# Kernel optimization log

Measured on AMD Instinct MI355X. Metric: run time of the kernel, lower is better.

## Reference

```python
import jax, jax.numpy as jnp
import numpy as np

B, S, DM, H, FF, BLOCK, R = 2, 4096, 768, 12, 3072, 64, 3
NB = S // BLOCK  # 64 blocks


def _layer_norm(x, g, b, eps=1e-5):
    mu = jnp.mean(x, -1, keepdims=True)
    var = jnp.var(x, -1, keepdims=True)
    return (x - mu) * jax.lax.rsqrt(var + eps) * g + b


def _bigbird_attn(x, rand_attn, Wq, bq, Wk, bk, Wv, bv):
    b_, s_, dm = x.shape
    h_ = H
    d = dm // h_
    n = s_ // BLOCK
    r = rand_attn.shape[-1]
    scale = 1.0 / np.sqrt(d).astype(np.float32)

    def heads(y):  # [B,S,DM] -> [B,H,n,block,D]
        return y.reshape(b_, s_, h_, d).transpose(0, 2, 1, 3).reshape(b_, h_, n, BLOCK, d)

    qb = heads(x @ Wq + bq)
    kb = heads(x @ Wk + bk)
    vb = heads(x @ Wv + bv)
    k_full = kb.reshape(b_, h_, s_, d)
    v_full = vb.reshape(b_, h_, s_, d)

    # gather random key/value blocks per head: [B,H,n-2,r*block,D]
    gather = jax.vmap(lambda zh, idx: zh[:, idx], in_axes=(1, 0), out_axes=1)
    gk = gather(kb, rand_attn).reshape(b_, h_, n - 2, r * BLOCK, d)
    gv = gather(vb, rand_attn).reshape(b_, h_, n - 2, r * BLOCK, d)

    def attend(q, k, v):
        s = jnp.einsum('...qd,...kd->...qk', q, k) * scale
        a = jax.nn.softmax(s, axis=-1)
        return jnp.einsum('...qk,...kd->...qd', a, v)

    # first block: full attention over all keys
    c_first = attend(qb[:, :, 0], k_full, v_full)

    # second block: blocks 0,1,2 + last block + random blocks
    k2 = jnp.concatenate([kb[:, :, 0], kb[:, :, 1], kb[:, :, 2], kb[:, :, -1], gk[:, :, 0]], axis=2)
    v2 = jnp.concatenate([vb[:, :, 0], vb[:, :, 1], vb[:, :, 2], vb[:, :, -1], gv[:, :, 0]], axis=2)
    c_second = attend(qb[:, :, 1], k2, v2)

    # middle blocks 2..n-3: global-first + 3-block sliding window + random + global-last
    m = n - 4
    qm = qb[:, :, 2:-2]  # [B,H,m,block,D]

    def band(z):  # sliding window of 3 blocks around each middle block
        return jnp.concatenate([z[:, :, 1:-3], z[:, :, 2:-2], z[:, :, 3:-1]], axis=3)

    bc = lambda z: jnp.broadcast_to(z[:, :, None], (b_, h_, m, BLOCK, d))
    km = jnp.concatenate([bc(kb[:, :, 0]), band(kb), gk[:, :, 1:-1], bc(kb[:, :, -1])], axis=3)
    vm = jnp.concatenate([bc(vb[:, :, 0]), band(vb), gv[:, :, 1:-1], bc(vb[:, :, -1])], axis=3)
    c_mid = attend(qm, km, vm)  # [B,H,m,block,D]

    # second-to-last block: block 0 + last three blocks + random blocks
    kp = jnp.concatenate([kb[:, :, 0], kb[:, :, -3], kb[:, :, -2], kb[:, :, -1], gk[:, :, -1]], axis=2)
    vp = jnp.concatenate([vb[:, :, 0], vb[:, :, -3], vb[:, :, -2], vb[:, :, -1], gv[:, :, -1]], axis=2)
    c_pen = attend(qb[:, :, -2], kp, vp)

    # last block: full attention over all keys
    c_last = attend(qb[:, :, -1], k_full, v_full)

    ctx = jnp.concatenate([c_first[:, :, None], c_second[:, :, None], c_mid,
                           c_pen[:, :, None], c_last[:, :, None]], axis=2)
    return ctx.reshape(b_, h_, s_, d).transpose(0, 2, 1, 3).reshape(b_, s_, dm)


def setup_inputs() -> dict:
    key = jax.random.key(0)
    ks = jax.random.split(key, 16)
    p = lambda k, shape: (jax.random.normal(k, shape, jnp.float32) * 0.02)
    return {
        'x': jax.random.normal(ks[0], (B, S, DM), jnp.float32),
        'rand_attn': jax.random.randint(ks[1], (H, NB - 2, R), 0, NB - 2, jnp.int32),
        'Wq': p(ks[2], (DM, DM)), 'bq': jnp.zeros((DM,), jnp.float32),
        'Wk': p(ks[3], (DM, DM)), 'bk': jnp.zeros((DM,), jnp.float32),
        'Wv': p(ks[4], (DM, DM)), 'bv': jnp.zeros((DM,), jnp.float32),
        'ln1_g': jnp.ones((DM,), jnp.float32), 'ln1_b': jnp.zeros((DM,), jnp.float32),
        'W1': p(ks[5], (DM, FF)), 'b1': jnp.zeros((FF,), jnp.float32),
        'W2': p(ks[6], (FF, DM)), 'b2': jnp.zeros((DM,), jnp.float32),
        'ln2_g': jnp.ones((DM,), jnp.float32), 'ln2_b': jnp.zeros((DM,), jnp.float32),
    }


def reference(x, rand_attn, Wq, bq, Wk, bk, Wv, bv, ln1_g, ln1_b, W1, b1, W2, b2, ln2_g, ln2_b):
    attn = _bigbird_attn(x, rand_attn, Wq, bq, Wk, bk, Wv, bv)
    h = _layer_norm(attn + x, ln1_g, ln1_b)  # dropout is identity in eval
    ffn = jax.nn.gelu(h @ W1 + b1, approximate=False) @ W2 + b2
    return _layer_norm(ffn + h, ln2_g, ln2_b)
```

## Files before the change

### kernel.cpp

```cpp
#include <hip/hip_runtime.h>
#include <cmath>


typedef unsigned short bf;
typedef __attribute__((ext_vector_type(8))) short bf16x8;
typedef __attribute__((ext_vector_type(4))) float f32x4;

__device__ __forceinline__ float bf2f(bf u) { return __uint_as_float(((unsigned)u) << 16); }
__device__ __forceinline__ bf f2bf(float f) {
  unsigned x = __float_as_uint(f);
  x += 0x7FFFu + ((x >> 16) & 1u);
  return (bf)(x >> 16);
}

__device__ __forceinline__ void gload16(const bf* g, char* lds) {
  __builtin_amdgcn_global_load_lds(
      (const __attribute__((address_space(1))) void*)g,
      (__attribute__((address_space(3))) void*)lds, 16, 0, 0);
}

__global__ __launch_bounds__(256) void cvt_x_k(const float* __restrict__ X,
                                               bf* __restrict__ xb)
{
  size_t i = ((size_t)blockIdx.x * 256 + threadIdx.x) * 8;
  float4 f0 = *(const float4*)&X[i];
  float4 f1 = *(const float4*)&X[i + 4];
  *(ushort4*)&xb[i]     = make_ushort4(f2bf(f0.x), f2bf(f0.y), f2bf(f0.z), f2bf(f0.w));
  *(ushort4*)&xb[i + 4] = make_ushort4(f2bf(f1.x), f2bf(f1.y), f2bf(f1.z), f2bf(f1.w));
}

__global__ __launch_bounds__(256) void tconv_k(const float* __restrict__ W,
                                               bf* __restrict__ Wt, int K, int N)
{
  __shared__ float tile[64][65];
  const int t = threadIdx.x;
  const int bn = blockIdx.x * 64, bk = blockIdx.y * 64;
  const int r = t >> 2, c0 = (t & 3) * 16;
  #pragma unroll
  for (int i = 0; i < 4; ++i) {
    float4 f = *(const float4*)&W[(size_t)(bk + r) * N + bn + c0 + i * 4];
    tile[r][c0 + i*4 + 0] = f.x; tile[r][c0 + i*4 + 1] = f.y;
    tile[r][c0 + i*4 + 2] = f.z; tile[r][c0 + i*4 + 3] = f.w;
  }
  __syncthreads();
  #pragma unroll
  for (int i = 0; i < 4; ++i) {
    int c = c0 + i * 4;
    ushort4 u = make_ushort4(f2bf(tile[c + 0][r]), f2bf(tile[c + 1][r]),
                             f2bf(tile[c + 2][r]), f2bf(tile[c + 3][r]));
    *(ushort4*)&Wt[(size_t)(bn + r) * K + bk + c] = u;
  }
}

template <int BN, typename TC>
__global__ __launch_bounds__(256) void gl_gemm_k(
    const bf* __restrict__ A, const bf* __restrict__ Bt,
    const float* __restrict__ bias, TC* __restrict__ C,
    int M, int N, int K, int ldbt, int ep)
{
  constexpr int NJ = BN / 32;
  __shared__ char smem[16384 + BN * 128];
  char* sA = smem;
  char* sB = smem + 16384;
  const int t = threadIdx.x;
  const int bm = blockIdx.y * 128, bn = blockIdx.x * BN;
  const int lane = t & 63, wid = t >> 6;
  const int wm = wid >> 1, wn = wid & 1;
  const int fr = lane & 15, fq = lane >> 4;
  const int lr = lane >> 3, lk = (lane & 7) * 8;

  f32x4 acc[4][NJ];
  #pragma unroll
  for (int i = 0; i < 4; ++i)
    #pragma unroll
    for (int j = 0; j < NJ; ++j) acc[i][j] = (f32x4){0.f, 0.f, 0.f, 0.f};

  for (int k0 = 0; k0 < K; k0 += 64) {
    #pragma unroll
    for (int c = 0; c < 4; ++c) {
      int chunk = wid * 4 + c;
      int row = chunk * 8 + lr;
      gload16(A + (size_t)(bm + row) * K + k0 + lk, sA + chunk * 1024);
    }
    #pragma unroll
    for (int c = 0; c < NJ; ++c) {
      int chunk = wid * NJ + c;
      int col = chunk * 8 + lr;
      gload16(Bt + (size_t)(bn + col) * ldbt + k0 + lk, sB + chunk * 1024);
    }
    __syncthreads();
    #pragma unroll
    for (int kk = 0; kk < 2; ++kk) {
      const int kb = kk * 64 + fq * 16;
      bf16x8 a[4], b[NJ];
      #pragma unroll
      for (int i = 0; i < 4; ++i)
        a[i] = *(const bf16x8*)(sA + (wm * 64 + i * 16 + fr) * 128 + kb);
      #pragma unroll
      for (int j = 0; j < NJ; ++j)
        b[j] = *(const bf16x8*)(sB + (wn * (BN / 2) + j * 16 + fr) * 128 + kb);
      #pragma unroll
      for (int i = 0; i < 4; ++i)
        #pragma unroll
        for (int j = 0; j < NJ; ++j)
          acc[i][j] = __builtin_amdgcn_mfma_f32_16x16x32_bf16(a[i], b[j], acc[i][j], 0, 0, 0);
    }
    __syncthreads();
  }
  #pragma unroll
  for (int j = 0; j < NJ; ++j) {
    int col = bn + wn * (BN / 2) + j * 16 + fr;
    float bias_v = bias ? bias[col] : 0.f;
    #pragma unroll
    for (int i = 0; i < 4; ++i) {
      int row0 = bm + wm * 64 + i * 16 + fq * 4;
      #pragma unroll
      for (int r = 0; r < 4; ++r) {
        float v = acc[i][j][r] + bias_v;
        if (ep == 1) v = 0.5f * v * (1.0f + erff(v * 0.70710678118654752f));
        if constexpr (sizeof(TC) == 2) C[(size_t)(row0 + r) * N + col] = f2bf(v);
        else                           C[(size_t)(row0 + r) * N + col] = v;
      }
    }
  }
}

__global__ __launch_bounds__(256) void qkv_gl_k(
    const bf* __restrict__ A, const bf* __restrict__ Bt,
    const float* __restrict__ bq, const float* __restrict__ bk,
    const float* __restrict__ bv,
    bf* __restrict__ Qo, bf* __restrict__ Ko, bf* __restrict__ Vo)
{
  __shared__ char smem[32768];
  char* sA = smem;
  char* sB = smem + 16384;
  const int t = threadIdx.x;
  const int bm = blockIdx.y * 128, bn = blockIdx.x * 128;
  const int lane = t & 63, wid = t >> 6;
  const int wm = wid >> 1, wn = wid & 1;
  const int fr = lane & 15, fq = lane >> 4;
  const int lr = lane >> 3, lk = (lane & 7) * 8;
  const int K = 768;

  f32x4 acc[4][4];
  #pragma unroll
  for (int i = 0; i < 4; ++i)
    #pragma unroll
    for (int j = 0; j < 4; ++j) acc[i][j] = (f32x4){0.f, 0.f, 0.f, 0.f};

  for (int k0 = 0; k0 < K; k0 += 64) {
    #pragma unroll
    for (int c = 0; c < 4; ++c) {
      int chunk = wid * 4 + c;
      gload16(A + (size_t)(bm + chunk * 8 + lr) * K + k0 + lk, sA + chunk * 1024);
    }
    #pragma unroll
    for (int c = 0; c < 4; ++c) {
      int chunk = wid * 4 + c;
      gload16(Bt + (size_t)(bn + chunk * 8 + lr) * K + k0 + lk, sB + chunk * 1024);
    }
    __syncthreads();
    #pragma unroll
    for (int kk = 0; kk < 2; ++kk) {
      const int kb = kk * 64 + fq * 16;
      bf16x8 a[4], b[4];
      #pragma unroll
      for (int i = 0; i < 4; ++i)
        a[i] = *(const bf16x8*)(sA + (wm * 64 + i * 16 + fr) * 128 + kb);
      #pragma unroll
      for (int j = 0; j < 4; ++j)
        b[j] = *(const bf16x8*)(sB + (wn * 64 + j * 16 + fr) * 128 + kb);
      #pragma unroll
      for (int i = 0; i < 4; ++i)
        #pragma unroll
        for (int j = 0; j < 4; ++j)
          acc[i][j] = __builtin_amdgcn_mfma_f32_16x16x32_bf16(a[i], b[j], acc[i][j], 0, 0, 0);
    }
    __syncthreads();
  }
  const int seg = bn / 768;
  const int cb  = bn - seg * 768;
  bf* dst = (seg == 0) ? Qo : ((seg == 1) ? Ko : Vo);
  const float* bias = (seg == 0) ? bq : ((seg == 1) ? bk : bv);
  #pragma unroll
  for (int j = 0; j < 4; ++j) {
    int col = cb + wn * 64 + j * 16 + fr;
    float bias_v = bias[col];
    #pragma unroll
    for (int i = 0; i < 4; ++i) {
      int row0 = bm + wm * 64 + i * 16 + fq * 4;
      #pragma unroll
      for (int r = 0; r < 4; ++r)
        dst[(size_t)(row0 + r) * 768 + col] = f2bf(acc[i][j][r] + bias_v);
    }
  }
}

__device__ __forceinline__ void stage_kv(char* bK, char* bVT,
    int kkey, int kd0, int vkey, int w,
    uint4 k0, uint4 k1, uint4 v0, uint4 v1)
{
  const int sw = (kkey & 7) << 4;
  *(uint4*)(bK + kkey * 128 + ((2 * kd0) ^ sw))      = k0;
  *(uint4*)(bK + kkey * 128 + ((2 * kd0 + 16) ^ sw)) = k1;
  union { uint4 q; unsigned short s[8]; } a, c;
  a.q = v0; c.q = v1;
  #pragma unroll
  for (int i = 0; i < 8; ++i) {
    int d = w * 16 + i;
    *(unsigned short*)(bVT + d * 128 + ((2 * vkey) ^ ((d & 7) << 4))) = a.s[i];
  }
  #pragma unroll
  for (int i = 0; i < 8; ++i) {
    int d = w * 16 + 8 + i;
    *(unsigned short*)(bVT + d * 128 + ((2 * vkey) ^ ((d & 7) << 4))) = c.s[i];
  }
}

__global__ __launch_bounds__(256) void attn5_kernel(
    const bf* __restrict__ Q, const bf* __restrict__ K,
    const bf* __restrict__ V, const int* __restrict__ rnd,
    float* __restrict__ ctx, float* __restrict__ part, int nseg)
{
  __shared__ char sQP[8192];
  __shared__ char sKV[2][16384];
  __shared__ int klist[8];
  const int t = threadIdx.x;
  const int lane = t & 63, w = t >> 6;
  const int fr = lane & 15, fq = lane >> 4;
  const int wg = blockIdx.x;
  const int nheavy = 48 * nseg;
  const bool heavy = wg < nheavy;
  int b, h, n, nkb, seg = 0, hidx = 0, segBase = 0;
  if (heavy) {
    hidx = wg / nseg; seg = wg - hidx * nseg;
    n = (hidx & 1) ? 63 : 0;
    int bh = hidx >> 1; h = bh % 12; b = bh / 12;
    nkb = 64 / nseg; segBase = seg * nkb;
  } else {
    int idx = wg - nheavy;
    n = 1 + (idx % 62);
    int bh = idx / 62; h = bh % 12; b = bh / 12;
    nkb = (n == 1 || n == 62) ? 7 : 8;
    if (t == 0) {
      int cnt = 0;
      if (n == 1)       { klist[0]=0; klist[1]=1;  klist[2]=2;  klist[3]=63; cnt=4; }
      else if (n == 62) { klist[0]=0; klist[1]=61; klist[2]=62; klist[3]=63; cnt=4; }
      else              { klist[0]=0; klist[1]=n-1; klist[2]=n; klist[3]=n+1; cnt=4; }
      for (int j = 0; j < 3; ++j) klist[cnt++] = rnd[(h * 62 + (n - 1)) * 3 + j];
      if (n != 1 && n != 62) klist[cnt++] = 63;
    }
  }
  const size_t qbase = ((size_t)b * 4096 + (size_t)n * 64) * 768 + h * 64;

  {
    int row = t >> 2, d0 = (t & 3) * 16;
    const bf* qp = &Q[qbase + (size_t)row * 768 + d0];
    #pragma unroll
    for (int i = 0; i < 2; ++i) {
      int off = row * 128 + ((2 * (d0 + 8 * i)) ^ ((row & 7) << 4));
      *(uint4*)(sQP + off) = *(const uint4*)(qp + 8 * i);
    }
  }
  __syncthreads();
  bf16x8 qf[2];
  {
    int row = w * 16 + fr;
    qf[0] = *(const bf16x8*)(sQP + row * 128 + ((2 * (fq * 8))      ^ ((row & 7) << 4)));
    qf[1] = *(const bf16x8*)(sQP + row * 128 + ((2 * (32 + fq * 8)) ^ ((row & 7) << 4)));
  }

  const int kkey = t >> 2, kd0 = (t & 3) * 16;
  const int vkey = lane;

  uint4 pk0, pk1, pv0, pv1;
  {
    int kb = heavy ? segBase : klist[0];
    size_t kbase = ((size_t)b * 4096 + (size_t)kb * 64) * 768 + h * 64;
    const bf* kp = &K[kbase + (size_t)kkey * 768 + kd0];
    pk0 = *(const uint4*)kp;  pk1 = *(const uint4*)(kp + 8);
    const bf* vp = &V[kbase + (size_t)vkey * 768 + w * 16];
    pv0 = *(const uint4*)vp;  pv1 = *(const uint4*)(vp + 8);
  }
  stage_kv(sKV[0], sKV[0] + 8192, kkey, kd0, vkey, w, pk0, pk1, pv0, pv1);

  float m_r[4] = {-1e30f, -1e30f, -1e30f, -1e30f};
  float l_r[4] = {0.f, 0.f, 0.f, 0.f};
  f32x4 acc_o[4];
  #pragma unroll
  for (int j = 0; j < 4; ++j) acc_o[j] = (f32x4){0.f, 0.f, 0.f, 0.f};

  for (int ib = 0; ib < nkb; ++ib) {
    char* bK  = sKV[ib & 1];
    char* bVT = bK + 8192;
    const bool pfv = (ib + 1 < nkb);
    if (pfv) {
      int kb = heavy ? (segBase + ib + 1) : klist[ib + 1];
      size_t kbase = ((size_t)b * 4096 + (size_t)kb * 64) * 768 + h * 64;
      const bf* kp = &K[kbase + (size_t)kkey * 768 + kd0];
      pk0 = *(const uint4*)kp;  pk1 = *(const uint4*)(kp + 8);
      const bf* vp = &V[kbase + (size_t)vkey * 768 + w * 16];
      pv0 = *(const uint4*)vp;  pv1 = *(const uint4*)(vp + 8);
    }
    __syncthreads();
    f32x4 s4[4];
    #pragma unroll
    for (int j = 0; j < 4; ++j) s4[j] = (f32x4){0.f, 0.f, 0.f, 0.f};
    __builtin_amdgcn_s_setprio(1);
    #pragma unroll
    for (int kk = 0; kk < 2; ++kk) {
      #pragma unroll
      for (int j = 0; j < 4; ++j) {
        int key = j * 16 + fr;
        bf16x8 kf = *(const bf16x8*)(bK + key * 128 + ((2 * (kk * 32 + fq * 8)) ^ ((key & 7) << 4)));
        s4[j] = __builtin_amdgcn_mfma_f32_16x16x32_bf16(qf[kk], kf, s4[j], 0, 0, 0);
      }
    }
    __builtin_amdgcn_s_setprio(0);
    #pragma unroll
    for (int j = 0; j < 4; ++j) s4[j] *= 0.125f;
    float c_r[4];
    #pragma unroll
    for (int r = 0; r < 4; ++r) {
      float mx = fmaxf(fmaxf(s4[0][r], s4[1][r]), fmaxf(s4[2][r], s4[3][r]));
      #pragma unroll
      for (int m = 1; m < 16; m <<= 1) mx = fmaxf(mx, __shfl_xor(mx, m, 64));
      float mn = fmaxf(mx, m_r[r]);
      float c  = __expf(m_r[r] - mn);
      float p0 = __expf(s4[0][r] - mn), p1 = __expf(s4[1][r] - mn);
      float p2 = __expf(s4[2][r] - mn), p3 = __expf(s4[3][r] - mn);
      s4[0][r] = p0; s4[1][r] = p1; s4[2][r] = p2; s4[3][r] = p3;
      float sum = p0 + p1 + p2 + p3;
      #pragma unroll
      for (int m = 1; m < 16; m <<= 1) sum += __shfl_xor(sum, m, 64);
      l_r[r] = l_r[r] * c + sum;
      m_r[r] = mn;
      c_r[r] = c;
    }
    #pragma unroll
    for (int j = 0; j < 4; ++j)
      #pragma unroll
      for (int r = 0; r < 4; ++r) acc_o[j][r] *= c_r[r];
    #pragma unroll
    for (int r = 0; r < 4; ++r) {
      int prow = w * 16 + fq * 4 + r;
      int rs = prow * 128, sw = (prow & 7) << 4;
      #pragma unroll
      for (int j = 0; j < 4; ++j)
        *(unsigned short*)(sQP + rs + ((2 * (j * 16 + fr)) ^ sw)) = f2bf(s4[j][r]);
    }
    if (pfv)
      stage_kv(sKV[(ib & 1) ^ 1], sKV[(ib & 1) ^ 1] + 8192, kkey, kd0, vkey, w,
               pk0, pk1, pv0, pv1);
    __builtin_amdgcn_s_setprio(1);
    #pragma unroll
    for (int kk = 0; kk < 2; ++kk) {
      int prow = w * 16 + fr;
      bf16x8 pf8 = *(const bf16x8*)(sQP + prow * 128 + ((2 * (kk * 32 + fq * 8)) ^ ((prow & 7) << 4)));
      #pragma unroll
      for (int j = 0; j < 4; ++j) {
        int col = j * 16 + fr;
        bf16x8 vf = *(const bf16x8*)(bVT + col * 128 + ((2 * (kk * 32 + fq * 8)) ^ ((col & 7) << 4)));
        acc_o[j] = __builtin_amdgcn_mfma_f32_16x16x32_bf16(pf8, vf, acc_o[j], 0, 0, 0);
      }
    }
    __builtin_amdgcn_s_setprio(0);
  }
  if (heavy && nseg > 1) {
    float* pb = part + ((size_t)hidx * nseg + seg) * 4224;
    int row0 = w * 16 + fq * 4;
    #pragma unroll
    for (int r = 0; r < 4; ++r) {
      int row = row0 + r;
      if (fr == 0) { pb[4096 + row] = m_r[r]; pb[4160 + row] = l_r[r]; }
      #pragma unroll
      for (int j = 0; j < 4; ++j)
        pb[row * 64 + j * 16 + fr] = acc_o[j][r];
    }
  } else {
    int row0 = w * 16 + fq * 4;
    #pragma unroll
    for (int r = 0; r < 4; ++r) {
      float inv = 1.f / l_r[r];
      size_t rowoff = qbase + (size_t)(row0 + r) * 768;
      #pragma unroll
      for (int j = 0; j < 4; ++j)
        ctx[rowoff + j * 16 + fr] = acc_o[j][r] * inv;
    }
  }
}

__global__ __launch_bounds__(256) void attn_combine_k(
    const float* __restrict__ part, float* __restrict__ ctx)
{
  const int hidx = blockIdx.x;
  const int t = threadIdx.x;
  const int n = (hidx & 1) ? 63 : 0;
  const int bh = hidx >> 1;
  const int h = bh % 12, b = bh / 12;
  const size_t qbase = ((size_t)b * 4096 + (size_t)n * 64) * 768 + h * 64;
  const int r = t >> 2, d0 = (t & 3) * 16;
  const float* pb = part + (size_t)hidx * 8 * 4224;
  float mi[8], li[8], m = -1e30f;
  #pragma unroll
  for (int i = 0; i < 8; ++i) {
    mi[i] = pb[i * 4224 + 4096 + r];
    li[i] = pb[i * 4224 + 4160 + r];
    m = fmaxf(m, mi[i]);
  }
  float w8[8], L = 0.f;
  #pragma unroll
  for (int i = 0; i < 8; ++i) { w8[i] = __expf(mi[i] - m); L += li[i] * w8[i]; }
  float inv = 1.f / L;
  #pragma unroll
  for (int dd = 0; dd < 4; ++dd) {
    int d = d0 + dd * 4;
    float4 o = {0.f, 0.f, 0.f, 0.f};
    #pragma unroll
    for (int i = 0; i < 8; ++i) {
      float4 p = *(const float4*)&pb[i * 4224 + r * 64 + d];
      o.x = fmaf(w8[i], p.x, o.x); o.y = fmaf(w8[i], p.y, o.y);
      o.z = fmaf(w8[i], p.z, o.z); o.w = fmaf(w8[i], p.w, o.w);
    }
    o.x *= inv; o.y *= inv; o.z *= inv; o.w *= inv;
    *(float4*)&ctx[qbase + (size_t)r * 768 + d] = o;
  }
}

template <typename TR, typename TO>
__global__ __launch_bounds__(256) void ln_kernel(
    const float* __restrict__ a, const TR* __restrict__ res,
    const float* __restrict__ g, const float* __restrict__ bb,
    TO* __restrict__ out)
{
  const int row = blockIdx.x, t = threadIdx.x;
  __shared__ float buf[768];
  __shared__ float rs[4], rss[4];
  const size_t base = (size_t)row * 768;
  float s = 0.f, ss = 0.f;
  for (int c = t; c < 768; c += 256) {
    float rv;
    if constexpr (sizeof(TR) == 2) rv = bf2f(res[base + c]);
    else                           rv = res[base + c];
    float v = a[base + c] + rv;
    buf[c] = v;
    s += v;
    ss = fmaf(v, v, ss);
  }
  #pragma unroll
  for (int off = 32; off > 0; off >>= 1) {
    s  += __shfl_down(s, off, 64);
    ss += __shfl_down(ss, off, 64);
  }
  if ((t & 63) == 0) { rs[t >> 6] = s; rss[t >> 6] = ss; }
  __syncthreads();
  float S  = rs[0] + rs[1] + rs[2] + rs[3];
  float SS = rss[0] + rss[1] + rss[2] + rss[3];
  float mu  = S * (1.f / 768.f);
  float var = SS * (1.f / 768.f) - mu * mu;
  float inv = rsqrtf(var + 1e-5f);
  for (int c = t; c < 768; c += 256) {
    float v = (buf[c] - mu) * inv * g[c] + bb[c];
    if constexpr (sizeof(TO) == 2) out[base + c] = f2bf(v);
    else                           out[base + c] = v;
  }
}

extern "C" void kernel_launch(void* const* d_in, const int* in_sizes, int n_in,
                              void* d_out, int out_size, void* d_ws, size_t ws_size,
                              hipStream_t stream)
{
  const float* x   = (const float*)d_in[0];
  const int*   rnd = (const int*)d_in[1];
  const float* Wq  = (const float*)d_in[2];
  const float* bq  = (const float*)d_in[3];
  const float* Wk  = (const float*)d_in[4];
  const float* bk  = (const float*)d_in[5];
  const float* Wv  = (const float*)d_in[6];
  const float* bv  = (const float*)d_in[7];
  const float* g1  = (const float*)d_in[8];
  const float* be1 = (const float*)d_in[9];
  const float* W1  = (const float*)d_in[10];
  const float* b1  = (const float*)d_in[11];
  const float* W2  = (const float*)d_in[12];
  const float* b2  = (const float*)d_in[13];
  const float* g2  = (const float*)d_in[14];
  const float* be2 = (const float*)d_in[15];
  float* out = (float*)d_out;

  char* W = (char*)d_ws;
  bf* w1t   = (bf*)(W);
  bf* w2t   = (bf*)(W + 4718592);
  bf* Kb    = (bf*)(W + 9437184);
  bf* wqkv  = (bf*)(W + 22020096);
  bf* xb    = (bf*)(W + 25559040);
  bf* Qb    = (bf*)(W + 38141952);
  bf* Vb    = (bf*)(W + 50724864);
  float* part = (float*)(W + 63307776);
  bf* f1    = (bf*)(W + 22020096);
  bf* h1    = Kb;
  float* ctx = out;
  float* f2  = out;

  dim3 blk(256);
  cvt_x_k<<<dim3(3072), blk, 0, stream>>>(x, xb);
  tconv_k<<<dim3(12, 12), blk, 0, stream>>>(Wq, wqkv,               768, 768);
  tconv_k<<<dim3(12, 12), blk, 0, stream>>>(Wk, wqkv + 589824,      768, 768);
  tconv_k<<<dim3(12, 12), blk, 0, stream>>>(Wv, wqkv + 2 * 589824,  768, 768);
  tconv_k<<<dim3(48, 12), blk, 0, stream>>>(W1, w1t,  768, 3072);
  tconv_k<<<dim3(12, 48), blk, 0, stream>>>(W2, w2t, 3072,  768);
  qkv_gl_k<<<dim3(18, 64), blk, 0, stream>>>(xb, wqkv, bq, bk, bv, Qb, Kb, Vb);
  attn5_kernel<<<dim3(48 * 8 + 2 * 12 * 62), blk, 0, stream>>>(
      Qb, Kb, Vb, rnd, ctx, part, 8);
  attn_combine_k<<<dim3(48), blk, 0, stream>>>(part, ctx);
  ln_kernel<float, bf><<<dim3(8192), blk, 0, stream>>>(ctx, x, g1, be1, h1);
  gl_gemm_k<128, bf><<<dim3(24, 64), blk, 0, stream>>>(
      h1, w1t, b1, f1, 8192, 3072, 768, 768, 1);
  gl_gemm_k<64, float><<<dim3(12, 64), blk, 0, stream>>>(
      f1, w2t, b2, f2, 8192, 768, 3072, 3072, 0);
  ln_kernel<bf, float><<<dim3(8192), blk, 0, stream>>>(f2, h1, g2, be2, out);
}
```

Measured before the change: 330.6 us.

## Double-buffer LDS in GEMM kernels and widen the W2 GEMM tile

Both GEMM kernels (the generic one and the fused QKV projection) now keep two LDS stages. The global-to-LDS load for the next K tile is issued before the MFMA work on the current tile, with one waitcnt and barrier per iteration instead of two syncthreads. Priority is raised around the MFMA block, and sched_barriers keep the compiler from reordering across stages. The FFN down-projection also switches from BN=64 to BN=128, halving its grid to 384 blocks, which trades fewer redundant A loads for lower occupancy and parallelism.

New measurement: 301.2 us. -8.9%, faster.

```diff
diff --git a/kernel.cpp b/kernel.cpp
--- a/kernel.cpp
+++ b/kernel.cpp
@@ -59,9 +59,9 @@
     int M, int N, int K, int ldbt, int ep)
 {
   constexpr int NJ = BN / 32;
-  __shared__ char smem[16384 + BN * 128];
-  char* sA = smem;
-  char* sB = smem + 16384;
+  constexpr int ASZ = 16384;
+  constexpr int BSZ = BN * 128;
+  __shared__ char smem[2 * (ASZ + BSZ)];
   const int t = threadIdx.x;
   const int bm = blockIdx.y * 128, bn = blockIdx.x * BN;
   const int lane = t & 63, wid = t >> 6;
@@ -75,20 +75,33 @@
     #pragma unroll
     for (int j = 0; j < NJ; ++j) acc[i][j] = (f32x4){0.f, 0.f, 0.f, 0.f};
 
-  for (int k0 = 0; k0 < K; k0 += 64) {
+  auto STAGE = [&](int p, int k0) {
+    char* sA = smem + p * (ASZ + BSZ);
+    char* sB = sA + ASZ;
     #pragma unroll
     for (int c = 0; c < 4; ++c) {
       int chunk = wid * 4 + c;
-      int row = chunk * 8 + lr;
-      gload16(A + (size_t)(bm + row) * K + k0 + lk, sA + chunk * 1024);
+      gload16(A + (size_t)(bm + chunk * 8 + lr) * K + k0 + lk, sA + chunk * 1024);
     }
     #pragma unroll
     for (int c = 0; c < NJ; ++c) {
       int chunk = wid * NJ + c;
-      int col = chunk * 8 + lr;
-      gload16(Bt + (size_t)(bn + col) * ldbt + k0 + lk, sB + chunk * 1024);
-    }
-    __syncthreads();
+      gload16(Bt + (size_t)(bn + chunk * 8 + lr) * ldbt + k0 + lk, sB + chunk * 1024);
+    }
+  };
+
+  const int T = K >> 6;
+  STAGE(0, 0);
+  asm volatile("s_waitcnt vmcnt(0)" ::: "memory");
+  __builtin_amdgcn_s_barrier();
+  __builtin_amdgcn_sched_barrier(0);
+  int cur = 0;
+  for (int tt = 0; tt < T; ++tt) {
+    if (tt + 1 < T) STAGE(cur ^ 1, (tt + 1) * 64);
+    __builtin_amdgcn_sched_barrier(0);
+    char* sA = smem + cur * (ASZ + BSZ);
+    char* sB = sA + ASZ;
+    __builtin_amdgcn_s_setprio(1);
     #pragma unroll
     for (int kk = 0; kk < 2; ++kk) {
       const int kb = kk * 64 + fq * 16;
@@ -105,7 +118,12 @@
         for (int j = 0; j < NJ; ++j)
           acc[i][j] = __builtin_amdgcn_mfma_f32_16x16x32_bf16(a[i], b[j], acc[i][j], 0, 0, 0);
     }
-    __syncthreads();
+    __builtin_amdgcn_s_setprio(0);
+    __builtin_amdgcn_sched_barrier(0);
+    asm volatile("s_waitcnt vmcnt(0)" ::: "memory");
+    __builtin_amdgcn_s_barrier();
+    __builtin_amdgcn_sched_barrier(0);
+    cur ^= 1;
   }
   #pragma unroll
   for (int j = 0; j < NJ; ++j) {
@@ -131,9 +149,8 @@
     const float* __restrict__ bv,
     bf* __restrict__ Qo, bf* __restrict__ Ko, bf* __restrict__ Vo)
 {
-  __shared__ char smem[32768];
-  char* sA = smem;
-  char* sB = smem + 16384;
+  constexpr int ASZ = 16384, BSZ = 16384;
+  __shared__ char smem[2 * (ASZ + BSZ)];
   const int t = threadIdx.x;
   const int bm = blockIdx.y * 128, bn = blockIdx.x * 128;
   const int lane = t & 63, wid = t >> 6;
@@ -148,7 +165,9 @@
     #pragma unroll
     for (int j = 0; j < 4; ++j) acc[i][j] = (f32x4){0.f, 0.f, 0.f, 0.f};
 
-  for (int k0 = 0; k0 < K; k0 += 64) {
+  auto STAGE = [&](int p, int k0) {
+    char* sA = smem + p * (ASZ + BSZ);
+    char* sB = sA + ASZ;
     #pragma unroll
     for (int c = 0; c < 4; ++c) {
       int chunk = wid * 4 + c;
@@ -159,7 +178,19 @@
       int chunk = wid * 4 + c;
       gload16(Bt + (size_t)(bn + chunk * 8 + lr) * K + k0 + lk, sB + chunk * 1024);
     }
-    __syncthreads();
+  };
+
+  STAGE(0, 0);
+  asm volatile("s_waitcnt vmcnt(0)" ::: "memory");
+  __builtin_amdgcn_s_barrier();
+  __builtin_amdgcn_sched_barrier(0);
+  int cur = 0;
+  for (int tt = 0; tt < 12; ++tt) {
+    if (tt + 1 < 12) STAGE(cur ^ 1, (tt + 1) * 64);
+    __builtin_amdgcn_sched_barrier(0);
+    char* sA = smem + cur * (ASZ + BSZ);
+    char* sB = sA + ASZ;
+    __builtin_amdgcn_s_setprio(1);
     #pragma unroll
     for (int kk = 0; kk < 2; ++kk) {
       const int kb = kk * 64 + fq * 16;
@@ -176,7 +207,12 @@
         for (int j = 0; j < 4; ++j)
           acc[i][j] = __builtin_amdgcn_mfma_f32_16x16x32_bf16(a[i], b[j], acc[i][j], 0, 0, 0);
     }
-    __syncthreads();
+    __builtin_amdgcn_s_setprio(0);
+    __builtin_amdgcn_sched_barrier(0);
+    asm volatile("s_waitcnt vmcnt(0)" ::: "memory");
+    __builtin_amdgcn_s_barrier();
+    __builtin_amdgcn_sched_barrier(0);
+    cur ^= 1;
   }
   const int seg = bn / 768;
   const int cb  = bn - seg * 768;
@@ -516,7 +552,7 @@
   ln_kernel<float, bf><<<dim3(8192), blk, 0, stream>>>(ctx, x, g1, be1, h1);
   gl_gemm_k<128, bf><<<dim3(24, 64), blk, 0, stream>>>(
       h1, w1t, b1, f1, 8192, 3072, 768, 768, 1);
-  gl_gemm_k<64, float><<<dim3(12, 64), blk, 0, stream>>>(
+  gl_gemm_k<128, float><<<dim3(6, 64), blk, 0, stream>>>(
       f1, w2t, b2, f2, 8192, 768, 3072, 3072, 0);
   ln_kernel<bf, float><<<dim3(8192), blk, 0, stream>>>(f2, h1, g2, be2, out);
 }
```

## Unify GEMMs into triple-buffered swizzled kernel with 128x64 tiles

Applied to the files above, without the earlier changes.

Replaces the separate QKV and generic GEMM kernels with one templated kernel. It uses a three-stage LDS ring buffer fed by async global-to-LDS loads, with explicit vmcnt waits and a single barrier per k-step. Both the LDS layout and the reads are XOR-swizzled to avoid bank conflicts, and s_setprio is raised around the MFMA section. All GEMMs now use 128x64 tiles, so the QKV and FFN1 grids double in size. The intent is to hide global load latency and reduce LDS conflicts, at the cost of more LDS per block and more A-tile reloads due to the narrower N tiles.

Result: faster. 309.7 us (-6.3%).

```diff
diff --git a/kernel.cpp b/kernel.cpp
--- a/kernel.cpp
+++ b/kernel.cpp
@@ -52,146 +52,119 @@
   }
 }
 
-template <int BN, typename TC>
-__global__ __launch_bounds__(256) void gl_gemm_k(
+template <int QKVMODE, typename TC>
+__global__ __launch_bounds__(256) void gl3_gemm_k(
     const bf* __restrict__ A, const bf* __restrict__ Bt,
-    const float* __restrict__ bias, TC* __restrict__ C,
+    const float* __restrict__ b0p, const float* __restrict__ b1p,
+    const float* __restrict__ b2p,
+    TC* __restrict__ C0, bf* __restrict__ C1, bf* __restrict__ C2,
     int M, int N, int K, int ldbt, int ep)
 {
-  constexpr int NJ = BN / 32;
-  __shared__ char smem[16384 + BN * 128];
-  char* sA = smem;
-  char* sB = smem + 16384;
+  constexpr int BUF = 24576;
+  __shared__ char smem[3 * BUF];
   const int t = threadIdx.x;
-  const int bm = blockIdx.y * 128, bn = blockIdx.x * BN;
+  const int bm = blockIdx.y * 128, bn = blockIdx.x * 64;
   const int lane = t & 63, wid = t >> 6;
   const int wm = wid >> 1, wn = wid & 1;
   const int fr = lane & 15, fq = lane >> 4;
-  const int lr = lane >> 3, lk = (lane & 7) * 8;
-
-  f32x4 acc[4][NJ];
+
+  f32x4 acc[4][2];
   #pragma unroll
   for (int i = 0; i < 4; ++i)
     #pragma unroll
-    for (int j = 0; j < NJ; ++j) acc[i][j] = (f32x4){0.f, 0.f, 0.f, 0.f};
-
-  for (int k0 = 0; k0 < K; k0 += 64) {
+    for (int j = 0; j < 2; ++j) acc[i][j] = (f32x4){0.f, 0.f, 0.f, 0.f};
+
+  auto STAGE = [&](int p, int k0) {
+    char* sA = smem + p * BUF;
+    char* sB = sA + 16384;
     #pragma unroll
     for (int c = 0; c < 4; ++c) {
-      int chunk = wid * 4 + c;
-      int row = chunk * 8 + lr;
-      gload16(A + (size_t)(bm + row) * K + k0 + lk, sA + chunk * 1024);
-    }
-    #pragma unroll
-    for (int c = 0; c < NJ; ++c) {
-      int chunk = wid * NJ + c;
-      int col = chunk * 8 + lr;
-      gload16(Bt + (size_t)(bn + col) * ldbt + k0 + lk, sB + chunk * 1024);
-    }
-    __syncthreads();
+      int idx = c * 256 + t;
+      int row = idx >> 3, ks = idx & 7;
+      gload16(A + (size_t)(bm + row) * K + k0 + ((ks ^ (row & 7)) << 3),
+              sA + (c * 256 + wid * 64) * 16);
+    }
+    #pragma unroll
+    for (int c = 0; c < 2; ++c) {
+      int idx = c * 256 + t;
+      int row = idx >> 3, ks = idx & 7;
+      gload16(Bt + (size_t)(bn + row) * ldbt + k0 + ((ks ^ (row & 7)) << 3),
+              sB + (c * 256 + wid * 64) * 16);
+    }
+  };
+
+  const int T = K >> 6;
+  STAGE(0, 0);
+  STAGE(1, 64);
+  asm volatile("s_waitcnt vmcnt(6)" ::: "memory");
+  __builtin_amdgcn_s_barrier();
+  __builtin_amdgcn_sched_barrier(0);
+  for (int tt = 0; tt < T; ++tt) {
+    if (tt + 2 < T) STAGE((tt + 2) % 3, (tt + 2) * 64);
+    __builtin_amdgcn_sched_barrier(0);
+    char* sA = smem + (tt % 3) * BUF;
+    char* sB = sA + 16384;
+    __builtin_amdgcn_s_setprio(1);
     #pragma unroll
     for (int kk = 0; kk < 2; ++kk) {
       const int kb = kk * 64 + fq * 16;
-      bf16x8 a[4], b[NJ];
-      #pragma unroll
-      for (int i = 0; i < 4; ++i)
-        a[i] = *(const bf16x8*)(sA + (wm * 64 + i * 16 + fr) * 128 + kb);
-      #pragma unroll
-      for (int j = 0; j < NJ; ++j)
-        b[j] = *(const bf16x8*)(sB + (wn * (BN / 2) + j * 16 + fr) * 128 + kb);
+      bf16x8 a[4], b[2];
+      #pragma unroll
+      for (int i = 0; i < 4; ++i) {
+        int row = wm * 64 + i * 16 + fr;
+        a[i] = *(const bf16x8*)(sA + row * 128 + (kb ^ ((row & 7) << 4)));
+      }
+      #pragma unroll
+      for (int j = 0; j < 2; ++j) {
+        int col = wn * 32 + j * 16 + fr;
+        b[j] = *(const bf16x8*)(sB + col * 128 + (kb ^ ((col & 7) << 4)));
+      }
       #pragma unroll
       for (int i = 0; i < 4; ++i)
         #pragma unroll
-        for (int j = 0; j < NJ; ++j)
+        for (int j = 0; j < 2; ++j)
           acc[i][j] = __builtin_amdgcn_mfma_f32_16x16x32_bf16(a[i], b[j], acc[i][j], 0, 0, 0);
     }
-    __syncthreads();
-  }
-  #pragma unroll
-  for (int j = 0; j < NJ; ++j) {
-    int col = bn + wn * (BN / 2) + j * 16 + fr;
-    float bias_v = bias ? bias[col] : 0.f;
-    #pragma unroll
-    for (int i = 0; i < 4; ++i) {
-      int row0 = bm + wm * 64 + i * 16 + fq * 4;
-      #pragma unroll
-      for (int r = 0; r < 4; ++r) {
-        float v = acc[i][j][r] + bias_v;
-        if (ep == 1) v = 0.5f * v * (1.0f + erff(v * 0.70710678118654752f));
-        if constexpr (sizeof(TC) == 2) C[(size_t)(row0 + r) * N + col] = f2bf(v);
-        else                           C[(size_t)(row0 + r) * N + col] = v;
-      }
-    }
-  }
-}
-
-__global__ __launch_bounds__(256) void qkv_gl_k(
-    const bf* __restrict__ A, const bf* __restrict__ Bt,
-    const float* __restrict__ bq, const float* __restrict__ bk,
-    const float* __restrict__ bv,
-    bf* __restrict__ Qo, bf* __restrict__ Ko, bf* __restrict__ Vo)
-{
-  __shared__ char smem[32768];
-  char* sA = smem;
-  char* sB = smem + 16384;
-  const int t = threadIdx.x;
-  const int bm = blockIdx.y * 128, bn = blockIdx.x * 128;
-  const int lane = t & 63, wid = t >> 6;
-  const int wm = wid >> 1, wn = wid & 1;
-  const int fr = lane & 15, fq = lane >> 4;
-  const int lr = lane >> 3, lk = (lane & 7) * 8;
-  const int K = 768;
-
-  f32x4 acc[4][4];
-  #pragma unroll
-  for (int i = 0; i < 4; ++i)
-    #pragma unroll
-    for (int j = 0; j < 4; ++j) acc[i][j] = (f32x4){0.f, 0.f, 0.f, 0.f};
-
-  for (int k0 = 0; k0 < K; k0 += 64) {
-    #pragma unroll
-    for (int c = 0; c < 4; ++c) {
-      int chunk = wid * 4 + c;
-      gload16(A + (size_t)(bm + chunk * 8 + lr) * K + k0 + lk, sA + chunk * 1024);
-    }
-    #pragma unroll
-    for (int c = 0; c < 4; ++c) {
-      int chunk = wid * 4 + c;
-      gload16(Bt + (size_t)(bn + chunk * 8 + lr) * K + k0 + lk, sB + chunk * 1024);
-    }
-    __syncthreads();
-    #pragma unroll
-    for (int kk = 0; kk < 2; ++kk) {
-      const int kb = kk * 64 + fq * 16;
-      bf16x8 a[4], b[4];
-      #pragma unroll
-      for (int i = 0; i < 4; ++i)
-        a[i] = *(const bf16x8*)(sA + (wm * 64 + i * 16 + fr) * 128 + kb);
-      #pragma unroll
-      for (int j = 0; j < 4; ++j)
-        b[j] = *(const bf16x8*)(sB + (wn * 64 + j * 16 + fr) * 128 + kb);
-      #pragma unroll
-      for (int i = 0; i < 4; ++i)
+    __builtin_amdgcn_s_setprio(0);
+    __builtin_amdgcn_sched_barrier(0);
+    if (tt + 2 < T) { asm volatile("s_waitcnt vmcnt(6)" ::: "memory"); }
+    else            { asm volatile("s_waitcnt vmcnt(0)" ::: "memory"); }
+    __builtin_amdgcn_s_barrier();
+    __builtin_amdgcn_sched_barrier(0);
+  }
+  if constexpr (QKVMODE) {
+    const int seg = bn / 768;
+    const int cb  = bn - seg * 768;
+    bf* dst = (seg == 0) ? (bf*)C0 : ((seg == 1) ? C1 : C2);
+    const float* bias = (seg == 0) ? b0p : ((seg == 1) ? b1p : b2p);
+    #pragma unroll
+    for (int j = 0; j < 2; ++j) {
+      int col = cb + wn * 32 + j * 16 + fr;
+      float bias_v = bias[col];
+      #pragma unroll
+      for (int i = 0; i < 4; ++i) {
+        int row0 = bm + wm * 64 + i * 16 + fq * 4;
         #pragma unroll
-        for (int j = 0; j < 4; ++j)
-          acc[i][j] = __builtin_amdgcn_mfma_f32_16x16x32_bf16(a[i], b[j], acc[i][j], 0, 0, 0);
-    }
-    __syncthreads();
-  }
-  const int seg = bn / 768;
-  const int cb  = bn - seg * 768;
-  bf* dst = (seg == 0) ? Qo : ((seg == 1) ? Ko : Vo);
-  const float* bias = (seg == 0) ? bq : ((seg == 1) ? bk : bv);
-  #pragma unroll
-  for (int j = 0; j < 4; ++j) {
-    int col = cb + wn * 64 + j * 16 + fr;
-    float bias_v = bias[col];
-    #pragma unroll
-    for (int i = 0; i < 4; ++i) {
-      int row0 = bm + wm * 64 + i * 16 + fq * 4;
-      #pragma unroll
-      for (int r = 0; r < 4; ++r)
-        dst[(size_t)(row0 + r) * 768 + col] = f2bf(acc[i][j][r] + bias_v);
+        for (int r = 0; r < 4; ++r)
+          dst[(size_t)(row0 + r) * 768 + col] = f2bf(acc[i][j][r] + bias_v);
+      }
+    }
+  } else {
+    #pragma unroll
+    for (int j = 0; j < 2; ++j) {
+      int col = bn + wn * 32 + j * 16 + fr;
+      float bias_v = b0p ? b0p[col] : 0.f;
+      #pragma unroll
+      for (int i = 0; i < 4; ++i) {
+        int row0 = bm + wm * 64 + i * 16 + fq * 4;
+        #pragma unroll
+        for (int r = 0; r < 4; ++r) {
+          float v = acc[i][j][r] + bias_v;
+          if (ep == 1) v = 0.5f * v * (1.0f + erff(v * 0.70710678118654752f));
+          if constexpr (sizeof(TC) == 2) C0[(size_t)(row0 + r) * N + col] = f2bf(v);
+          else                           C0[(size_t)(row0 + r) * N + col] = v;
+        }
+      }
     }
   }
 }
@@ -509,14 +482,15 @@
   tconv_k<<<dim3(12, 12), blk, 0, stream>>>(Wv, wqkv + 2 * 589824,  768, 768);
   tconv_k<<<dim3(48, 12), blk, 0, stream>>>(W1, w1t,  768, 3072);
   tconv_k<<<dim3(12, 48), blk, 0, stream>>>(W2, w2t, 3072,  768);
-  qkv_gl_k<<<dim3(18, 64), blk, 0, stream>>>(xb, wqkv, bq, bk, bv, Qb, Kb, Vb);
+  gl3_gemm_k<1, bf><<<dim3(36, 64), blk, 0, stream>>>(
+      xb, wqkv, bq, bk, bv, Qb, Kb, Vb, 8192, 2304, 768, 768, 0);
   attn5_kernel<<<dim3(48 * 8 + 2 * 12 * 62), blk, 0, stream>>>(
       Qb, Kb, Vb, rnd, ctx, part, 8);
   attn_combine_k<<<dim3(48), blk, 0, stream>>>(part, ctx);
   ln_kernel<float, bf><<<dim3(8192), blk, 0, stream>>>(ctx, x, g1, be1, h1);
-  gl_gemm_k<128, bf><<<dim3(24, 64), blk, 0, stream>>>(
-      h1, w1t, b1, f1, 8192, 3072, 768, 768, 1);
-  gl_gemm_k<64, float><<<dim3(12, 64), blk, 0, stream>>>(
-      f1, w2t, b2, f2, 8192, 768, 3072, 3072, 0);
+  gl3_gemm_k<0, bf><<<dim3(48, 64), blk, 0, stream>>>(
+      h1, w1t, b1, nullptr, nullptr, f1, nullptr, nullptr, 8192, 3072, 768, 768, 1);
+  gl3_gemm_k<0, float><<<dim3(12, 64), blk, 0, stream>>>(
+      f1, w2t, b2, nullptr, nullptr, f2, nullptr, nullptr, 8192, 768, 3072, 3072, 0);
   ln_kernel<bf, float><<<dim3(8192), blk, 0, stream>>>(f2, h1, g2, be2, out);
 }
```
